# Kernel tuning notes

Measured on AMD Instinct MI355X. Metric: run time of the kernel, lower is better.

Reference implementation:

```python
import jax, jax.numpy as jnp
import numpy as np

MUL = 16            # multiplicity of 0e and 1o in irreps_in/irreps_out
N_NODES = 12500
N_EDGES = 200000
EDGE_ATTR_DIM = 16
WEIGHT_NUMEL = 4 * MUL * MUL  # 4 uvw paths, mul_sh = 1


def setup_inputs() -> dict:
    key = jax.random.key(0)
    ks = jax.random.split(key, 8)
    node_attr = jax.random.normal(ks[0], (N_NODES, 4 * MUL), dtype=jnp.float32)
    edge_index = jax.random.randint(ks[1], (2, N_EDGES), 0, N_NODES, dtype=jnp.int64)
    edge_attr = jax.random.normal(ks[2], (N_EDGES, EDGE_ATTR_DIM), dtype=jnp.float32)
    edge_sh = jax.random.normal(ks[3], (N_EDGES, 4), dtype=jnp.float32)
    # radial ScalarMLP params: Linear(16,16) + SiLU + Linear(16, weight_numel)
    s1 = 1.0 / np.sqrt(EDGE_ATTR_DIM)
    w1 = jax.random.uniform(ks[4], (EDGE_ATTR_DIM, EDGE_ATTR_DIM), jnp.float32, -s1, s1)
    b1 = jax.random.uniform(ks[5], (EDGE_ATTR_DIM,), jnp.float32, -s1, s1)
    w2 = jax.random.uniform(ks[6], (EDGE_ATTR_DIM, WEIGHT_NUMEL), jnp.float32, -s1, s1)
    b2 = jax.random.uniform(ks[7], (WEIGHT_NUMEL,), jnp.float32, -s1, s1)
    return {"node_attr": node_attr, "edge_index": edge_index, "edge_attr": edge_attr,
            "edge_sh": edge_sh, "w1": w1, "b1": b1, "w2": w2, "b2": b2}


def _conv(node_attr, edge_index, edge_attr, edge_sh, w1, b1, w2, b2):
    N = node_attr.shape[0]
    E = edge_attr.shape[0]
    src, dst = edge_index[0], edge_index[1]

    # gather source node features per edge
    x = node_attr[src]                         # [E, 4*MUL]
    x0 = x[:, :MUL]                            # [E, MUL]    (16x0e)
    x1 = x[:, MUL:].reshape(E, MUL, 3)         # [E, MUL, 3] (16x1o)
    y0 = edge_sh[:, 0]                         # [E]   (1x0e)
    y1 = edge_sh[:, 1:4]                       # [E,3] (1x1o)

    # radial MLP -> per-edge tensor-product weights
    h = jax.nn.silu(edge_attr @ w1 + b1)
    W = (h @ w2 + b2).reshape(E, 4, MUL, MUL)  # 4 uvw paths, [E,4,u,w]

    alpha = 1.0 / np.sqrt(2 * MUL).astype(np.float32)  # path norm: 2 paths * MUL fan-in per out irrep
    inv_sqrt3 = np.float32(1.0 / np.sqrt(3.0))

    # path 0: 0e x 0e -> 0e (CG = 1)
    out0 = jnp.einsum('eu,euw->ew', x0 * y0[:, None], W[:, 0])
    # path 1: 1o x 1o -> 0e (CG = delta_ij / sqrt(3), component-normalized)
    out0 = out0 + inv_sqrt3 * jnp.einsum('eui,ei,euw->ew', x1, y1, W[:, 1])
    # path 2: 0e x 1o -> 1o (CG = identity)
    out1 = jnp.einsum('eu,ei,euw->ewi', x0, y1, W[:, 2])
    # path 3: 1o x 0e -> 1o (CG = identity)
    out1 = out1 + jnp.einsum('eui,e,euw->ewi', x1, y0, W[:, 3])

    out_ij = jnp.concatenate([alpha * out0, (alpha * out1).reshape(E, 3 * MUL)], axis=-1)

    # scatter-mean into destination nodes
    sums = jax.ops.segment_sum(out_ij, dst, num_segments=N)
    counts = jax.ops.segment_sum(jnp.ones((E,), out_ij.dtype), dst, num_segments=N)
    return sums / jnp.maximum(counts, 1.0)[:, None]


def reference(node_attr, edge_index, edge_attr, edge_sh, w1, b1, w2, b2):
    return _conv(node_attr, edge_index, edge_attr, edge_sh, w1, b1, w2, b2)
```

## Files before the change

### kernel.cpp

```cpp
#include <hip/hip_runtime.h>
#include <math.h>

#define E_TOTAL  200000
#define NNODES   12500
#define OUT_ELEM 800000
#define NTILE    (E_TOTAL / 64)
#define PAD      64

typedef float    f32x4 __attribute__((ext_vector_type(4)));
typedef _Float16 f16x8 __attribute__((ext_vector_type(8)));
typedef _Float16 f16x4 __attribute__((ext_vector_type(4)));
typedef _Float16 f16x2 __attribute__((ext_vector_type(2)));

union AF { f16x8 f; f16x2 h2[4]; };

static const size_t OFF_CNT    = (size_t)E_TOTAL * 64 * 2;
static const size_t OFF_POS    = OFF_CNT + (size_t)NNODES * 4;
static const size_t OFF_BFRAG  = (OFF_POS + (size_t)NNODES * PAD * 4 + 15) & ~(size_t)15;
static const size_t WS_NEEDED  = OFF_BFRAG + (size_t)36 * 64 * 8 * 2;

__global__ void k_prep(const float* __restrict__ w2, const float* __restrict__ b2,
                       int* __restrict__ cnt, _Float16* __restrict__ bfrag) {
    const int g = blockIdx.x * 256 + threadIdx.x;
    if (g < NNODES) cnt[g] = 0;
    if (g < 36 * 64) {
        const int slot = g >> 6, lane = g & 63;
        const int br = slot / 9, kb = slot - br * 9;
        const int quad = lane >> 4, n = lane & 15;
        const float alpha = 0.17677669529663687f;
        _Float16* dst = bfrag + (size_t)g * 8;
        #pragma unroll
        for (int j = 0; j < 8; ++j) {
            float v;
            if (kb < 8) {
                const int ku = kb * 32 + quad * 8 + j;
                v = w2[(ku >> 4) * 1024 + br * 256 + (ku & 15) * 16 + n];
            } else {
                const int loc = quad * 8 + j;
                v = (loc < 16) ? b2[br * 256 + loc * 16 + n] : 0.0f;
            }
            dst[j] = (_Float16)(alpha * v);
        }
    }
}

__global__ __launch_bounds__(256) void k_conv(
        const float* __restrict__ node_attr,
        const int*   __restrict__ edge_index,
        const float* __restrict__ edge_attr,
        const float* __restrict__ edge_sh,
        const float* __restrict__ w1,
        const float* __restrict__ b1,
        const f16x8* __restrict__ bfrag,
        int* __restrict__ cnt,
        int* __restrict__ pos,
        _Float16* __restrict__ edge_out)
{
    const int t = threadIdx.x;
    __shared__ float  sh_h[64][17];
    __shared__ float4 sh_y[64];
    __shared__ _Float16 sh_s[6][64][24];

    const int ebase = blockIdx.x * 64;
    const float inv_sqrt3 = 0.57735026918962576f;

    if (t < 64) {
        const int e2 = ebase + t;
        const int d = edge_index[E_TOTAL + e2];
        int slot = atomicAdd(&cnt[d], 1);
        if (slot >= PAD) slot = PAD - 1;
        pos[d * PAD + slot] = e2;
    }

    {
        const int e_loc = t & 63, kq = t >> 6;
        const int e = ebase + e_loc;
        const float* ea = edge_attr + (size_t)e * 16;
        float ear[16];
        #pragma unroll
        for (int dq = 0; dq < 4; ++dq) {
            float4 v = *(const float4*)(ea + dq * 4);
            ear[dq * 4 + 0] = v.x; ear[dq * 4 + 1] = v.y;
            ear[dq * 4 + 2] = v.z; ear[dq * 4 + 3] = v.w;
        }
        float4 acc = *(const float4*)(b1 + kq * 4);
        #pragma unroll
        for (int d = 0; d < 16; ++d) {
            float4 wr = *(const float4*)(w1 + d * 16 + kq * 4);
            acc.x += ear[d] * wr.x; acc.y += ear[d] * wr.y;
            acc.z += ear[d] * wr.z; acc.w += ear[d] * wr.w;
        }
        sh_h[e_loc][kq * 4 + 0] = acc.x / (1.0f + __expf(-acc.x));
        sh_h[e_loc][kq * 4 + 1] = acc.y / (1.0f + __expf(-acc.y));
        sh_h[e_loc][kq * 4 + 2] = acc.z / (1.0f + __expf(-acc.z));
        sh_h[e_loc][kq * 4 + 3] = acc.w / (1.0f + __expf(-acc.w));
    }

    {
        const int e_loc = (t & 15) + ((t >> 6) << 4);
        const int pp = (t >> 4) & 3;
        const int u0 = pp * 4;
        const int e = ebase + e_loc;
        const int src = edge_index[e];
        const float4 yv = *(const float4*)(edge_sh + (size_t)e * 4);
        const float* xp = node_attr + (size_t)src * 64;
        float4 x0v = *(const float4*)(xp + u0);
        float x1v[4][3];
        #pragma unroll
        for (int q = 0; q < 4; ++q)
            #pragma unroll
            for (int i = 0; i < 3; ++i)
                x1v[q][i] = xp[16 + (u0 + q) * 3 + i];
        const float* x0p = &x0v.x;
        f16x4 s0h, s1h, x0h, ah, bh, ch;
        #pragma unroll
        for (int q = 0; q < 4; ++q) {
            s0h[q] = (_Float16)(x0p[q] * yv.x);
            s1h[q] = (_Float16)(inv_sqrt3 * (x1v[q][0] * yv.y + x1v[q][1] * yv.z + x1v[q][2] * yv.w));
            x0h[q] = (_Float16)x0p[q];
            ah[q]  = (_Float16)x1v[q][0];
            bh[q]  = (_Float16)x1v[q][1];
            ch[q]  = (_Float16)x1v[q][2];
        }
        *(f16x4*)&sh_s[0][e_loc][u0] = s0h;
        *(f16x4*)&sh_s[1][e_loc][u0] = s1h;
        *(f16x4*)&sh_s[2][e_loc][u0] = x0h;
        *(f16x4*)&sh_s[3][e_loc][u0] = ah;
        *(f16x4*)&sh_s[4][e_loc][u0] = bh;
        *(f16x4*)&sh_s[5][e_loc][u0] = ch;
        if (pp == 0) sh_y[e_loc] = yv;
    }
    __syncthreads();

    const int lane = t & 63, wv = t >> 6;
    const int m = lane & 15, quad = lane >> 4;
    const int e_loc = wv * 16 + m;
    const int qh = quad >> 1, ql = quad & 1;

    AF svh[6];
    #pragma unroll
    for (int b = 0; b < 6; ++b)
        svh[b].f = *(const f16x8*)&sh_s[b][e_loc][ql * 8];
    float hreg[8];
    #pragma unroll
    for (int kb = 0; kb < 8; ++kb) hreg[kb] = sh_h[e_loc][2 * kb + qh];

    f32x4 acc0  = {0.f, 0.f, 0.f, 0.f};
    f32x4 acc2  = {0.f, 0.f, 0.f, 0.f};
    f32x4 acc3a = {0.f, 0.f, 0.f, 0.f};
    f32x4 acc3b = {0.f, 0.f, 0.f, 0.f};
    f32x4 acc3c = {0.f, 0.f, 0.f, 0.f};

    for (int kb = 0; kb < 9; ++kb) {
        const f16x8 B0 = bfrag[(0 * 9 + kb) * 64 + lane];
        const f16x8 B1 = bfrag[(1 * 9 + kb) * 64 + lane];
        const f16x8 B2 = bfrag[(2 * 9 + kb) * 64 + lane];
        const f16x8 B3 = bfrag[(3 * 9 + kb) * 64 + lane];
        const float selF = (kb < 8) ? hreg[kb] : ((quad < 2) ? 1.0f : 0.0f);
        const _Float16 sh1 = (_Float16)selF;
        const f16x2 sel2 = (f16x2){sh1, sh1};
        AF A[6];
        #pragma unroll
        for (int b = 0; b < 6; ++b)
            #pragma unroll
            for (int p = 0; p < 4; ++p)
                A[b].h2[p] = sel2 * svh[b].h2[p];
        acc0  = __builtin_amdgcn_mfma_f32_16x16x32_f16(A[0].f, B0, acc0, 0, 0, 0);
        acc0  = __builtin_amdgcn_mfma_f32_16x16x32_f16(A[1].f, B1, acc0, 0, 0, 0);
        acc2  = __builtin_amdgcn_mfma_f32_16x16x32_f16(A[2].f, B2, acc2, 0, 0, 0);
        acc3a = __builtin_amdgcn_mfma_f32_16x16x32_f16(A[3].f, B3, acc3a, 0, 0, 0);
        acc3b = __builtin_amdgcn_mfma_f32_16x16x32_f16(A[4].f, B3, acc3b, 0, 0, 0);
        acc3c = __builtin_amdgcn_mfma_f32_16x16x32_f16(A[5].f, B3, acc3c, 0, 0, 0);
    }

    #pragma unroll
    for (int r = 0; r < 4; ++r) {
        const int el = wv * 16 + quad * 4 + r;
        const float4 yv = sh_y[el];
        const float t2v = acc2[r];
        const float o0 = acc0[r];
        const float oa = yv.y * t2v + yv.x * acc3a[r];
        const float ob = yv.z * t2v + yv.x * acc3b[r];
        const float oc = yv.w * t2v + yv.x * acc3c[r];
        f16x4 pk = {(_Float16)o0, (_Float16)oa, (_Float16)ob, (_Float16)oc};
        *(f16x4*)(edge_out + (size_t)(ebase + el) * 64 + m * 4) = pk;
    }
}

__global__ __launch_bounds__(256) void k_gather(const _Float16* __restrict__ edge_out,
                                                const int* __restrict__ cnt,
                                                const int* __restrict__ pos,
                                                float* __restrict__ out) {
    const int t = threadIdx.x;
    const int lane = t & 63;
    const int n = blockIdx.x * 4 + (t >> 6);
    int pe;
    if (lane < 16) pe = lane * 4;
    else { const int idx = lane - 16; const int w = idx / 3; pe = w * 4 + 1 + (idx - w * 3); }
    int c = cnt[n];
    if (c > PAD) c = PAD;
    const int p = (lane < c) ? pos[n * PAD + lane] : 0;
    float a0 = 0.f, a1 = 0.f, a2 = 0.f, a3 = 0.f;
    int j = 0;
    for (; j + 4 <= c; j += 4) {
        const int r0 = __shfl(p, j + 0);
        const int r1 = __shfl(p, j + 1);
        const int r2 = __shfl(p, j + 2);
        const int r3 = __shfl(p, j + 3);
        a0 += (float)edge_out[(size_t)r0 * 64 + pe];
        a1 += (float)edge_out[(size_t)r1 * 64 + pe];
        a2 += (float)edge_out[(size_t)r2 * 64 + pe];
        a3 += (float)edge_out[(size_t)r3 * 64 + pe];
    }
    for (; j < c; ++j) {
        const int r = __shfl(p, j);
        a0 += (float)edge_out[(size_t)r * 64 + pe];
    }
    const float acc = (a0 + a1) + (a2 + a3);
    out[n * 64 + lane] = acc / (c > 0 ? (float)c : 1.0f);
}

__global__ void k_zero_f(float* __restrict__ out, float* __restrict__ counts) {
    int i = blockIdx.x * 256 + threadIdx.x;
    if (i < OUT_ELEM) out[i] = 0.0f;
    if (i < NNODES)   counts[i] = 0.0f;
}

#define EPB 80
#define NE  8
__global__ __launch_bounds__(256) void k_conv_atomic(
        const float* __restrict__ node_attr,
        const int*   __restrict__ edge_index,
        const float* __restrict__ edge_attr,
        const float* __restrict__ edge_sh,
        const float* __restrict__ w1,
        const float* __restrict__ b1,
        const float* __restrict__ w2,
        const float* __restrict__ b2,
        float* __restrict__ out,
        float* __restrict__ counts)
{
    const int thr   = threadIdx.x;
    const int lane  = thr & 63;
    const int wv    = thr >> 6;
    const int u     = lane >> 2;
    const int wbase = (lane & 3) * 4;

    float4 w2r[16];
    #pragma unroll
    for (int k = 0; k < 16; ++k)
        w2r[k] = *(const float4*)(w2 + k * 1024 + thr * 4);
    const float4 b2r = *(const float4*)(b2 + thr * 4);

    __shared__ __align__(16) float sh_h[NE][16];
    __shared__ float sh_s0[NE][16];
    __shared__ float sh_s1[NE][16];
    __shared__ float sh_x0[NE][16];
    __shared__ float sh_x1[NE][16][3];
    __shared__ float sh_y0[NE];
    __shared__ float sh_y1[NE][3];
    __shared__ int   sh_dst[NE];

    const float alpha     = 0.17677669529663687f;
    const float inv_sqrt3 = 0.57735026918962576f;
    const int e0 = blockIdx.x * EPB;

    for (int batch = 0; batch < EPB / NE; ++batch) {
        const int ebase = e0 + batch * NE;
        if (thr < 128) {
            const int le = thr >> 4, k = thr & 15;
            const int e = ebase + le;
            float acc = b1[k];
            const float* ea = edge_attr + (size_t)e * 16;
            #pragma unroll
            for (int d = 0; d < 16; ++d) acc += ea[d] * w1[d * 16 + k];
            sh_h[le][k] = acc / (1.0f + __expf(-acc));
            if (k == 0) sh_dst[le] = edge_index[E_TOTAL + e];
        } else {
            const int le = (thr - 128) >> 4, uu = thr & 15;
            const int e = ebase + le;
            const int src = edge_index[e];
            const float y0  = edge_sh[e * 4 + 0];
            const float y1a = edge_sh[e * 4 + 1];
            const float y1b = edge_sh[e * 4 + 2];
            const float y1c = edge_sh[e * 4 + 3];
            const float* xp = node_attr + (size_t)src * 64;
            const float x0v = xp[uu];
            const float xa = xp[16 + uu * 3 + 0];
            const float xb = xp[16 + uu * 3 + 1];
            const float xc = xp[16 + uu * 3 + 2];
            sh_x0[le][uu] = x0v;
            sh_x1[le][uu][0] = xa; sh_x1[le][uu][1] = xb; sh_x1[le][uu][2] = xc;
            sh_s0[le][uu] = x0v * y0;
            sh_s1[le][uu] = inv_sqrt3 * (xa * y1a + xb * y1b + xc * y1c);
            if (uu == 0) {
                sh_y0[le] = y0;
                sh_y1[le][0] = y1a; sh_y1[le][1] = y1b; sh_y1[le][2] = y1c;
            }
        }
        __syncthreads();

        for (int le = 0; le < NE; ++le) {
            float W0 = b2r.x, W1 = b2r.y, W2c = b2r.z, W3c = b2r.w;
            const float4* hv = (const float4*)sh_h[le];
            #pragma unroll
            for (int kk = 0; kk < 4; ++kk) {
                const float4 h4 = hv[kk];
                const int kb = kk * 4;
                W0  += h4.x * w2r[kb + 0].x; W1  += h4.x * w2r[kb + 0].y;
                W2c += h4.x * w2r[kb + 0].z; W3c += h4.x * w2r[kb + 0].w;
                W0  += h4.y * w2r[kb + 1].x; W1  += h4.y * w2r[kb + 1].y;
                W2c += h4.y * w2r[kb + 1].z; W3c += h4.y * w2r[kb + 1].w;
                W0  += h4.z * w2r[kb + 2].x; W1  += h4.z * w2r[kb + 2].y;
                W2c += h4.z * w2r[kb + 2].z; W3c += h4.z * w2r[kb + 2].w;
                W0  += h4.w * w2r[kb + 3].x; W1  += h4.w * w2r[kb + 3].y;
                W2c += h4.w * w2r[kb + 3].z; W3c += h4.w * w2r[kb + 3].w;
            }
            const int dst = sh_dst[le];
            float* op = out + (size_t)dst * 64;
            if (wv == 0 || wv == 1) {
                const float s = (wv == 0) ? sh_s0[le][u] : sh_s1[le][u];
                float v0 = s * W0, v1 = s * W1, v2 = s * W2c, v3 = s * W3c;
                #pragma unroll
                for (int off = 4; off <= 32; off <<= 1) {
                    v0 += __shfl_xor(v0, off); v1 += __shfl_xor(v1, off);
                    v2 += __shfl_xor(v2, off); v3 += __shfl_xor(v3, off);
                }
                if (lane < 4) {
                    atomicAdd(op + wbase + 0, alpha * v0);
                    atomicAdd(op + wbase + 1, alpha * v1);
                    atomicAdd(op + wbase + 2, alpha * v2);
                    atomicAdd(op + wbase + 3, alpha * v3);
                    if (wv == 0 && lane == 0) atomicAdd(&counts[dst], 1.0f);
                }
            } else if (wv == 2) {
                const float s = sh_x0[le][u];
                float v0 = s * W0, v1 = s * W1, v2 = s * W2c, v3 = s * W3c;
                #pragma unroll
                for (int off = 4; off <= 32; off <<= 1) {
                    v0 += __shfl_xor(v0, off); v1 += __shfl_xor(v1, off);
                    v2 += __shfl_xor(v2, off); v3 += __shfl_xor(v3, off);
                }
                if (lane < 4) {
                    const float ya = alpha * sh_y1[le][0];
                    const float yb = alpha * sh_y1[le][1];
                    const float yc = alpha * sh_y1[le][2];
                    float vv[4] = {v0, v1, v2, v3};
                    #pragma unroll
                    for (int q = 0; q < 4; ++q) {
                        float* qp = op + 16 + (wbase + q) * 3;
                        atomicAdd(qp + 0, vv[q] * ya);
                        atomicAdd(qp + 1, vv[q] * yb);
                        atomicAdd(qp + 2, vv[q] * yc);
                    }
                }
            } else {
                const float ay0 = alpha * sh_y0[le];
                #pragma unroll
                for (int i = 0; i < 3; ++i) {
                    const float s = sh_x1[le][u][i];
                    float v0 = s * W0, v1 = s * W1, v2 = s * W2c, v3 = s * W3c;
                    #pragma unroll
                    for (int off = 4; off <= 32; off <<= 1) {
                        v0 += __shfl_xor(v0, off); v1 += __shfl_xor(v1, off);
                        v2 += __shfl_xor(v2, off); v3 += __shfl_xor(v3, off);
                    }
                    if (lane < 4) {
                        atomicAdd(op + 16 + (wbase + 0) * 3 + i, ay0 * v0);
                        atomicAdd(op + 16 + (wbase + 1) * 3 + i, ay0 * v1);
                        atomicAdd(op + 16 + (wbase + 2) * 3 + i, ay0 * v2);
                        atomicAdd(op + 16 + (wbase + 3) * 3 + i, ay0 * v3);
                    }
                }
            }
        }
        __syncthreads();
    }
}

__global__ void k_div(float* __restrict__ out, const float* __restrict__ counts) {
    int i = blockIdx.x * 256 + threadIdx.x;
    if (i < OUT_ELEM) {
        float c = counts[i >> 6];
        out[i] *= 1.0f / fmaxf(c, 1.0f);
    }
}

extern "C" void kernel_launch(void* const* d_in, const int* in_sizes, int n_in,
                              void* d_out, int out_size, void* d_ws, size_t ws_size,
                              hipStream_t stream) {
    const float* node_attr  = (const float*)d_in[0];
    const int*   edge_index = (const int*)d_in[1];
    const float* edge_attr  = (const float*)d_in[2];
    const float* edge_sh    = (const float*)d_in[3];
    const float* w1         = (const float*)d_in[4];
    const float* b1         = (const float*)d_in[5];
    const float* w2         = (const float*)d_in[6];
    const float* b2         = (const float*)d_in[7];
    float* out = (float*)d_out;

    if (ws_size >= WS_NEEDED) {
        char* ws = (char*)d_ws;
        _Float16* edge_out = (_Float16*)ws;
        int*      cnt      = (int*)(ws + OFF_CNT);
        int*      pos      = (int*)(ws + OFF_POS);
        _Float16* bfrag    = (_Float16*)(ws + OFF_BFRAG);

        k_prep<<<(NNODES + 255) / 256, 256, 0, stream>>>(w2, b2, cnt, bfrag);
        k_conv<<<NTILE, 256, 0, stream>>>(
            node_attr, edge_index, edge_attr, edge_sh, w1, b1,
            (const f16x8*)bfrag, cnt, pos, edge_out);
        k_gather<<<NNODES / 4, 256, 0, stream>>>(edge_out, cnt, pos, out);
    } else {
        float* counts = (float*)d_ws;
        k_zero_f<<<(OUT_ELEM + 255) / 256, 256, 0, stream>>>(out, counts);
        k_conv_atomic<<<E_TOTAL / EPB, 256, 0, stream>>>(
            node_attr, edge_index, edge_attr, edge_sh, w1, b1, w2, b2, out, counts);
        k_div<<<(OUT_ELEM + 255) / 256, 256, 0, stream>>>(out, counts);
    }
}
```

Measured before the change: 126.0 us.

## Write edge outputs into per-node slot buckets for contiguous vectorized gather

The conv kernel now writes each edge's fp16 result directly to a per-destination-node bucket row (node*PAD+slot) instead of edge order, which removes the pos index array. The gather kernel then reads each node's bucket contiguously with 16-byte vector loads and reduces across lanes with shuffles and shared memory, replacing the scattered shfl-indexed per-element loads. This trades a larger workspace (NNODES*64 rows of 128 bytes) and scattered writes in conv for coalesced reads in gather. If the workspace is too small, the code falls back to the atomic path.

```diff
diff --git a/kernel.cpp b/kernel.cpp
--- a/kernel.cpp
+++ b/kernel.cpp
@@ -14,9 +14,8 @@
 
 union AF { f16x8 f; f16x2 h2[4]; };
 
-static const size_t OFF_CNT    = (size_t)E_TOTAL * 64 * 2;
-static const size_t OFF_POS    = OFF_CNT + (size_t)NNODES * 4;
-static const size_t OFF_BFRAG  = (OFF_POS + (size_t)NNODES * PAD * 4 + 15) & ~(size_t)15;
+static const size_t OFF_CNT    = (size_t)NNODES * PAD * 64 * 2;
+static const size_t OFF_BFRAG  = (OFF_CNT + (size_t)NNODES * 4 + 15) & ~(size_t)15;
 static const size_t WS_NEEDED  = OFF_BFRAG + (size_t)36 * 64 * 8 * 2;
 
 __global__ void k_prep(const float* __restrict__ w2, const float* __restrict__ b2,
@@ -53,13 +52,13 @@
         const float* __restrict__ b1,
         const f16x8* __restrict__ bfrag,
         int* __restrict__ cnt,
-        int* __restrict__ pos,
         _Float16* __restrict__ edge_out)
 {
     const int t = threadIdx.x;
     __shared__ float  sh_h[64][17];
     __shared__ float4 sh_y[64];
     __shared__ _Float16 sh_s[6][64][24];
+    __shared__ int sh_row[64];
 
     const int ebase = blockIdx.x * 64;
     const float inv_sqrt3 = 0.57735026918962576f;
@@ -69,7 +68,7 @@
         const int d = edge_index[E_TOTAL + e2];
         int slot = atomicAdd(&cnt[d], 1);
         if (slot >= PAD) slot = PAD - 1;
-        pos[d * PAD + slot] = e2;
+        sh_row[t] = d * PAD + slot;
     }
 
     {
@@ -183,41 +182,48 @@
         const float ob = yv.z * t2v + yv.x * acc3b[r];
         const float oc = yv.w * t2v + yv.x * acc3c[r];
         f16x4 pk = {(_Float16)o0, (_Float16)oa, (_Float16)ob, (_Float16)oc};
-        *(f16x4*)(edge_out + (size_t)(ebase + el) * 64 + m * 4) = pk;
+        const size_t row = (size_t)sh_row[el];
+        *(f16x4*)(edge_out + row * 64 + m * 4) = pk;
     }
 }
 
 __global__ __launch_bounds__(256) void k_gather(const _Float16* __restrict__ edge_out,
                                                 const int* __restrict__ cnt,
-                                                const int* __restrict__ pos,
                                                 float* __restrict__ out) {
+    __shared__ float sh_sum[4][64];
     const int t = threadIdx.x;
     const int lane = t & 63;
-    const int n = blockIdx.x * 4 + (t >> 6);
+    const int wv = t >> 6;
+    const int n = blockIdx.x * 4 + wv;
     int pe;
     if (lane < 16) pe = lane * 4;
     else { const int idx = lane - 16; const int w = idx / 3; pe = w * 4 + 1 + (idx - w * 3); }
     int c = cnt[n];
     if (c > PAD) c = PAD;
-    const int p = (lane < c) ? pos[n * PAD + lane] : 0;
-    float a0 = 0.f, a1 = 0.f, a2 = 0.f, a3 = 0.f;
-    int j = 0;
-    for (; j + 4 <= c; j += 4) {
-        const int r0 = __shfl(p, j + 0);
-        const int r1 = __shfl(p, j + 1);
-        const int r2 = __shfl(p, j + 2);
-        const int r3 = __shfl(p, j + 3);
-        a0 += (float)edge_out[(size_t)r0 * 64 + pe];
-        a1 += (float)edge_out[(size_t)r1 * 64 + pe];
-        a2 += (float)edge_out[(size_t)r2 * 64 + pe];
-        a3 += (float)edge_out[(size_t)r3 * 64 + pe];
-    }
-    for (; j < c; ++j) {
-        const int r = __shfl(p, j);
-        a0 += (float)edge_out[(size_t)r * 64 + pe];
-    }
-    const float acc = (a0 + a1) + (a2 + a3);
-    out[n * 64 + lane] = acc / (c > 0 ? (float)c : 1.0f);
+    const int ng = (c + 7) >> 3;
+    const f16x8* base = (const f16x8*)(edge_out + (size_t)n * PAD * 64);
+    const int rsub = lane >> 3;
+    float acc[8] = {0.f, 0.f, 0.f, 0.f, 0.f, 0.f, 0.f, 0.f};
+    for (int g = 0; g < ng; ++g) {
+        const f16x8 v = base[g * 64 + lane];
+        const int r = g * 8 + rsub;
+        #pragma unroll
+        for (int i = 0; i < 8; ++i)
+            acc[i] += (r < c) ? (float)v[i] : 0.0f;
+    }
+    #pragma unroll
+    for (int i = 0; i < 8; ++i) {
+        acc[i] += __shfl_xor(acc[i], 8);
+        acc[i] += __shfl_xor(acc[i], 16);
+        acc[i] += __shfl_xor(acc[i], 32);
+    }
+    if (lane < 8) {
+        #pragma unroll
+        for (int i = 0; i < 8; ++i) sh_sum[wv][lane * 8 + i] = acc[i];
+    }
+    __syncthreads();
+    const float s = sh_sum[wv][pe];
+    out[n * 64 + lane] = s / (c > 0 ? (float)c : 1.0f);
 }
 
 __global__ void k_zero_f(float* __restrict__ out, float* __restrict__ counts) {
@@ -403,14 +409,13 @@
         char* ws = (char*)d_ws;
         _Float16* edge_out = (_Float16*)ws;
         int*      cnt      = (int*)(ws + OFF_CNT);
-        int*      pos      = (int*)(ws + OFF_POS);
         _Float16* bfrag    = (_Float16*)(ws + OFF_BFRAG);
 
         k_prep<<<(NNODES + 255) / 256, 256, 0, stream>>>(w2, b2, cnt, bfrag);
         k_conv<<<NTILE, 256, 0, stream>>>(
             node_attr, edge_index, edge_attr, edge_sh, w1, b1,
-            (const f16x8*)bfrag, cnt, pos, edge_out);
-        k_gather<<<NNODES / 4, 256, 0, stream>>>(edge_out, cnt, pos, out);
+            (const f16x8*)bfrag, cnt, edge_out);
+        k_gather<<<NNODES / 4, 256, 0, stream>>>(edge_out, cnt, out);
     } else {
         float* counts = (float*)d_ws;
         k_zero_f<<<(OUT_ELEM + 255) / 256, 256, 0, stream>>>(out, counts);
```

Result: slower. 134.9 us (+7.1%).
